# Kernel optimization log

Hardware: AMD Instinct MI355X
Metric: run time of the kernel (lower is better)

Reference implementation:

```python
import jax, jax.numpy as jnp
import numpy as np

N = 100000   # nodes
E = 1600000  # edges (avg degree 16)
D = 64       # out_channels (in_channels == out_channels, so no zero-padding step)
L = 2        # GatedGraphConv num_layers


def setup_inputs() -> dict:
    key = jax.random.key(0)
    ks = jax.random.split(key, 11)
    w = lambda k, shape: jax.random.normal(k, shape, jnp.float32) * 0.05
    return {
        "x": jax.random.normal(ks[0], (N, D), jnp.float32),
        "edge_index": jax.random.randint(ks[1], (2, E), 0, N, dtype=jnp.int64),
        "conv_w": w(ks[2], (L, D, D)),        # GatedGraphConv per-layer message weight
        "gru_w_ih": w(ks[3], (3 * D, D)),     # GRUCell input->hidden (r|z|n)
        "gru_w_hh": w(ks[4], (3 * D, D)),     # GRUCell hidden->hidden (r|z|n)
        "gru_b_ih": w(ks[5], (3 * D,)),
        "gru_b_hh": w(ks[6], (3 * D,)),
        "lin_w": w(ks[7], (D, D)),            # nn.Linear(out, out)
        "lin_b": w(ks[8], (D,)),
        "attn_w": w(ks[9], (1, D)),           # nn.Linear(out, 1)
        "attn_b": w(ks[10], (1,)),
    }


def reference(x, edge_index, conv_w, gru_w_ih, gru_w_hh, gru_b_ih, gru_b_hh,
              lin_w, lin_b, attn_w, attn_b):
    src, dst = edge_index[0], edge_index[1]
    h = x  # in_channels == out_channels -> no padding
    for i in range(L):
        m = h @ conv_w[i]  # [N, D] transformed messages
        # gather at source nodes, scatter-add into target nodes
        agg = jax.ops.segment_sum(m[src], dst, num_segments=N)  # [N, D]
        # GRUCell(agg, h)
        gi = agg @ gru_w_ih.T + gru_b_ih  # [N, 3D]
        gh = h @ gru_w_hh.T + gru_b_hh    # [N, 3D]
        i_r, i_z, i_n = jnp.split(gi, 3, axis=1)
        h_r, h_z, h_n = jnp.split(gh, 3, axis=1)
        r = jax.nn.sigmoid(i_r + h_r)
        z = jax.nn.sigmoid(i_z + h_z)
        n = jnp.tanh(i_n + r * h_n)
        h = (1.0 - z) * n + z * h
    y = jax.nn.relu(h) @ lin_w.T + lin_b                 # [N, D]
    attn = jax.nn.softmax(y @ attn_w.T + attn_b, axis=0) # [N, 1], softmax over nodes
    return (attn * y).sum(axis=0, keepdims=True)          # [1, D]
```

## Files before the change

kernel.cpp:

```cpp
#include <hip/hip_runtime.h>


typedef __attribute__((ext_vector_type(8))) short s8v;
typedef __attribute__((ext_vector_type(4))) float f32x4;

#define CSR_CAP 12288
#define HSTR 136
#define LSTR 72

__device__ __forceinline__ unsigned short f32_bf16_rn(float x) {
  unsigned u = __float_as_uint(x);
  u += 0x7FFF + ((u >> 16) & 1);
  return (unsigned short)(u >> 16);
}

__device__ __forceinline__ int wave_incl_scan(int v, int lane) {
#pragma unroll
  for (int d = 1; d < 64; d <<= 1) {
    int u = __shfl_up(v, d);
    if (lane >= d) v += u;
  }
  return v;
}

__device__ __forceinline__ int detect_is64(const int* ei, int E) {
  int nz = 0;
  int lim = (E < 512) ? E : 512;
  for (int i = threadIdx.x; i < lim; i += blockDim.x)
    nz |= (ei[2 * i + 1] != 0);
  return __syncthreads_or(nz) ? 0 : 1;
}

__device__ __forceinline__ void load_edge(const int* ei, int E, int is64,
                                          int e, int& s, int& d) {
  if (is64) { s = ei[2 * e]; d = ei[2 * (E + e)]; }
  else      { s = ei[e];     d = ei[E + e]; }
}

__global__ __launch_bounds__(256) void count_kernel(
    const int* __restrict__ ei, int E,
    int* __restrict__ G, int P, int perBlk, int NB) {
  __shared__ int hist[512];
  int tid = threadIdx.x, b = blockIdx.x;
  for (int i = tid; i < 512; i += 256) hist[i] = 0;
  int is64 = detect_is64(ei, E);
  __syncthreads();
  int e0 = b * perBlk, e1 = min(e0 + perBlk, E);
  for (int e = e0 + tid; e < e1; e += 256) {
    int s, d; load_edge(ei, E, is64, e, s, d);
    atomicAdd(&hist[d >> 8], 1);
  }
  __syncthreads();
  for (int i = tid; i < P; i += 256) G[i * NB + b] = hist[i];
}

__global__ __launch_bounds__(256) void scan2a(int* __restrict__ G,
                                              int* __restrict__ total, int NB) {
  __shared__ int wsum[4];
  int p = blockIdx.x, tid = threadIdx.x, lane = tid & 63, wv = tid >> 6;
  int v = G[p * NB + tid];
  int incl = wave_incl_scan(v, lane);
  if (lane == 63) wsum[wv] = incl;
  __syncthreads();
  if (tid == 0) {
    int a = wsum[0], b2 = wsum[1], c = wsum[2], d = wsum[3];
    total[p] = a + b2 + c + d;
    wsum[0] = 0; wsum[1] = a; wsum[2] = a + b2; wsum[3] = a + b2 + c;
  }
  __syncthreads();
  G[p * NB + tid] = incl - v + wsum[wv];
}

__global__ void scan2b(const int* __restrict__ total, int* __restrict__ partStart,
                       int P) {
  int lane = threadIdx.x;
  int running = 0;
  for (int base = 0; base < P; base += 64) {
    int idx = base + lane;
    int v = (idx < P) ? total[idx] : 0;
    int incl = wave_incl_scan(v, lane);
    int tot = __shfl(incl, 63);
    if (idx < P) partStart[idx] = running + incl - v;
    running += tot;
  }
  if (lane == 0) partStart[P] = running;
}

__global__ __launch_bounds__(256) void scatter_kernel(
    const int* __restrict__ ei, int E,
    const int* __restrict__ G, const int* __restrict__ partStart,
    int* __restrict__ bucket, int P, int perBlk, int NB) {
  __shared__ int cur[512];
  int tid = threadIdx.x, b = blockIdx.x;
  int is64 = detect_is64(ei, E);
  for (int i = tid; i < P; i += 256) cur[i] = partStart[i] + G[i * NB + b];
  __syncthreads();
  int e0 = b * perBlk, e1 = min(e0 + perBlk, E);
  for (int e = e0 + tid; e < e1; e += 256) {
    int s, d; load_edge(ei, E, is64, e, s, d);
    int pos = atomicAdd(&cur[d >> 8], 1);
    bucket[pos] = ((d & 255) << 17) | s;
  }
}

__global__ __launch_bounds__(256) void buildcsr_kernel(
    const int* __restrict__ partStart, const int* __restrict__ bucket,
    int* __restrict__ row_ptr, int* __restrict__ col, int N) {
  __shared__ int stage[CSR_CAP];
  __shared__ int hist[256];
  __shared__ int cur[256];
  __shared__ int wsum[4];
  int p = blockIdx.x, tid = threadIdx.x;
  int beg = partStart[p], end = partStart[p + 1];
  int cnt = end - beg;
  int base = p << 8;
  hist[tid] = 0;
  __syncthreads();
  bool staged = (cnt <= CSR_CAP);
  if (staged) {
    for (int i = tid; i < cnt; i += 256) {
      int v = bucket[beg + i];
      stage[i] = v;
      atomicAdd(&hist[(v >> 17) & 255], 1);
    }
  } else {
    for (int i = tid; i < cnt; i += 256)
      atomicAdd(&hist[(bucket[beg + i] >> 17) & 255], 1);
  }
  __syncthreads();
  int lane = tid & 63, wv = tid >> 6;
  int v = hist[tid];
  int incl = wave_incl_scan(v, lane);
  if (lane == 63) wsum[wv] = incl;
  __syncthreads();
  if (tid == 0) {
    int s0 = wsum[0], s1 = wsum[1], s2 = wsum[2];
    wsum[0] = 0; wsum[1] = s0; wsum[2] = s0 + s1; wsum[3] = s0 + s1 + s2;
  }
  __syncthreads();
  int excl = incl - v + wsum[wv];
  cur[tid] = beg + excl;
  if (base + tid < N) {
    if (tid == 0) row_ptr[base] = beg;
    row_ptr[base + tid + 1] = beg + excl + v;
  }
  __syncthreads();
  if (staged) {
    for (int i = tid; i < cnt; i += 256) {
      int v2 = stage[i];
      int pos = atomicAdd(&cur[(v2 >> 17) & 255], 1);
      col[pos] = v2 & 0x1FFFF;
    }
  } else {
    for (int i = tid; i < cnt; i += 256) {
      int v2 = bucket[beg + i];
      int pos = atomicAdd(&cur[(v2 >> 17) & 255], 1);
      col[pos] = v2 & 0x1FFFF;
    }
  }
}

__global__ void wprep_kernel(const float* __restrict__ conv_w,
                             const float* __restrict__ w_ih,
                             const float* __restrict__ whh,
                             const float* __restrict__ lin_w,
                             unsigned short* __restrict__ Bt,
                             unsigned short* __restrict__ Lt) {
  int idx = blockIdx.x * blockDim.x + threadIdx.x;
  if (idx < 65536) {
    int l = idx >> 15;
    int rr = idx & 32767;
    int c = rr >> 7, p = rr & 127;
    int g = c >> 6, ch = c & 63;
    float val = 0.f;
    if (p < 64) {
      int j = (g == 0) ? ch : (g == 1) ? 64 + ch : (g == 2) ? 128 + ch : -1;
      if (j >= 0) {
        const float* C = conv_w + l * 4096 + p * 64;
        const float* W = w_ih + j * 64;
#pragma unroll 8
        for (int k = 0; k < 64; k++) val += C[k] * W[k];
      }
    } else {
      int q = p - 64;
      if (g == 0)      val = whh[ch * 64 + q];
      else if (g == 1) val = whh[(64 + ch) * 64 + q];
      else if (g == 3) val = whh[(128 + ch) * 64 + q];
    }
    unsigned short hi = f32_bf16_rn(val);
    float fh = __uint_as_float((unsigned)hi << 16);
    unsigned short lo = f32_bf16_rn(val - fh);
    size_t base = (size_t)l * 65536;
    Bt[base + (size_t)c * 128 + p] = hi;
    Bt[base + 32768 + (size_t)c * 128 + p] = lo;
  } else if (idx < 65536 + 4096) {
    int i2 = idx - 65536;
    float val = lin_w[i2];
    unsigned short hi = f32_bf16_rn(val);
    float fh = __uint_as_float((unsigned)hi << 16);
    unsigned short lo = f32_bf16_rn(val - fh);
    Lt[i2] = hi;
    Lt[4096 + i2] = lo;
  }
}

__global__ __launch_bounds__(256) void cvt16_kernel(
    const float* __restrict__ in, unsigned short* __restrict__ out, int n8) {
  int idx = blockIdx.x * blockDim.x + threadIdx.x;
  if (idx >= n8) return;
  const float4* p = (const float4*)(in + (size_t)idx * 8);
  float4 v0 = p[0], v1 = p[1];
  uint4 o;
  o.x = (unsigned)f32_bf16_rn(v0.x) | ((unsigned)f32_bf16_rn(v0.y) << 16);
  o.y = (unsigned)f32_bf16_rn(v0.z) | ((unsigned)f32_bf16_rn(v0.w) << 16);
  o.z = (unsigned)f32_bf16_rn(v1.x) | ((unsigned)f32_bf16_rn(v1.y) << 16);
  o.w = (unsigned)f32_bf16_rn(v1.z) | ((unsigned)f32_bf16_rn(v1.w) << 16);
  *(uint4*)(out + (size_t)idx * 8) = o;
}

__device__ __forceinline__ void acc_u4(const uint4& r, float* a) {
  a[0] += __uint_as_float(r.x << 16);
  a[1] += __uint_as_float(r.x & 0xFFFF0000u);
  a[2] += __uint_as_float(r.y << 16);
  a[3] += __uint_as_float(r.y & 0xFFFF0000u);
  a[4] += __uint_as_float(r.z << 16);
  a[5] += __uint_as_float(r.z & 0xFFFF0000u);
  a[6] += __uint_as_float(r.w << 16);
  a[7] += __uint_as_float(r.w & 0xFFFF0000u);
}

__global__ __launch_bounds__(256, 2) void gemm_gru_kernel(
    const unsigned short* __restrict__ src16, const int* __restrict__ row_ptr,
    const int* __restrict__ col, const float* __restrict__ hin,
    float* __restrict__ hout, unsigned short* __restrict__ hb16,
    const unsigned short* __restrict__ bt,
    const float* __restrict__ b_ih, const float* __restrict__ b_hh,
    int N, int ntiles, int wb16) {
  __shared__ short Ahi[64 * HSTR];
  __shared__ short Alo[64 * LSTR];
  const int tid = threadIdx.x;
  const int lane = tid & 63, w = tid >> 6;
  const int l15 = lane & 15, ko = (lane >> 4) * 8;

  s8v Bh[4][4], Bl[4][4];
  {
    const int colc = 16 * w + l15;
#pragma unroll
    for (int c = 0; c < 4; c++)
#pragma unroll
      for (int kk = 0; kk < 4; kk++) {
        size_t o = (size_t)(64 * c + colc) * 128 + kk * 32 + ko;
        Bh[c][kk] = *(const s8v*)(bt + o);
        Bl[c][kk] = *(const s8v*)(bt + 32768 + o);
      }
  }
  const int ch = 16 * w + l15;
  const float br = b_ih[ch] + b_hh[ch];
  const float bz = b_ih[64 + ch] + b_hh[64 + ch];
  const float bin_ = b_ih[128 + ch];
  const float bhn = b_hh[128 + ch];
  const int q4 = (lane >> 4) * 4;
  const int g = tid >> 2, qc = tid & 3;

  for (int tile = blockIdx.x; tile < ntiles; tile += gridDim.x) {
    const int nb = tile * 64;
    const int node = nb + g;
    {
      float a[16];
#pragma unroll
      for (int i = 0; i < 16; i++) a[i] = 0.f;
      if (node < N) {
        int beg = row_ptr[node], end = row_ptr[node + 1];
        int e = beg;
        for (; e + 2 <= end; e += 2) {
          const unsigned short* b0 = src16 + (size_t)col[e] * 64 + qc * 16;
          const unsigned short* b1 = src16 + (size_t)col[e + 1] * 64 + qc * 16;
          uint4 r0 = *(const uint4*)b0;
          uint4 r1 = *(const uint4*)(b0 + 8);
          uint4 r2 = *(const uint4*)b1;
          uint4 r3 = *(const uint4*)(b1 + 8);
          acc_u4(r0, a); acc_u4(r1, a + 8);
          acc_u4(r2, a); acc_u4(r3, a + 8);
        }
        if (e < end) {
          const unsigned short* b0 = src16 + (size_t)col[e] * 64 + qc * 16;
          uint4 r0 = *(const uint4*)b0;
          uint4 r1 = *(const uint4*)(b0 + 8);
          acc_u4(r0, a); acc_u4(r1, a + 8);
        }
      }
      s8v sv0, sv1;
#pragma unroll
      for (int i = 0; i < 8; i++) {
        sv0[i] = (short)f32_bf16_rn(a[i]);
        sv1[i] = (short)f32_bf16_rn(a[8 + i]);
      }
      short* sh = &Ahi[g * HSTR + qc * 16];
      *(s8v*)sh = sv0;
      *(s8v*)(sh + 8) = sv1;
    }
    {
      f32x4 v[4];
      if (node < N) {
#pragma unroll
        for (int i = 0; i < 4; i++)
          v[i] = *(const f32x4*)(hin + (size_t)node * 64 + qc * 16 + 4 * i);
      } else {
#pragma unroll
        for (int i = 0; i < 4; i++) v[i] = (f32x4)(0.f);
      }
      s8v hv0, hv1, lv0, lv1;
#pragma unroll
      for (int i = 0; i < 8; i++) {
        float x0 = v[i >> 2][i & 3];
        float x1 = v[2 + (i >> 2)][i & 3];
        unsigned short hb0 = f32_bf16_rn(x0);
        unsigned short hb1 = f32_bf16_rn(x1);
        hv0[i] = (short)hb0;
        hv1[i] = (short)hb1;
        lv0[i] = (short)f32_bf16_rn(x0 - __uint_as_float((unsigned)hb0 << 16));
        lv1[i] = (short)f32_bf16_rn(x1 - __uint_as_float((unsigned)hb1 << 16));
      }
      short* hh = &Ahi[g * HSTR + 64 + qc * 16];
      *(s8v*)hh = hv0;
      *(s8v*)(hh + 8) = hv1;
      short* hl = &Alo[g * LSTR + qc * 16];
      *(s8v*)hl = lv0;
      *(s8v*)(hl + 8) = lv1;
    }
    __syncthreads();

    f32x4 acc[4][4];
#pragma unroll
    for (int m = 0; m < 4; m++)
#pragma unroll
      for (int c = 0; c < 4; c++) acc[m][c] = (f32x4)(0.f);

#pragma unroll
    for (int m = 0; m < 4; m++) {
      const short* arh = &Ahi[(16 * m + l15) * HSTR + ko];
      const short* arl = &Alo[(16 * m + l15) * LSTR + ko];
#pragma unroll
      for (int kk = 0; kk < 4; kk++) {
        s8v a_h = *(const s8v*)(arh + kk * 32);
#pragma unroll
        for (int c = 0; c < 4; c++) {
          acc[m][c] = __builtin_amdgcn_mfma_f32_16x16x32_bf16(a_h, Bh[c][kk], acc[m][c], 0, 0, 0);
          acc[m][c] = __builtin_amdgcn_mfma_f32_16x16x32_bf16(a_h, Bl[c][kk], acc[m][c], 0, 0, 0);
        }
        if (kk >= 2) {
          s8v a_l = *(const s8v*)(arl + (kk - 2) * 32);
#pragma unroll
          for (int c = 0; c < 4; c++)
            acc[m][c] = __builtin_amdgcn_mfma_f32_16x16x32_bf16(a_l, Bh[c][kk], acc[m][c], 0, 0, 0);
        }
      }
    }

#pragma unroll
    for (int m = 0; m < 4; m++) {
#pragma unroll
      for (int gg = 0; gg < 4; gg++) {
        int loc = 16 * m + q4 + gg;
        int nd = nb + loc;
        if (nd < N) {
          unsigned hi = (unsigned short)Ahi[loc * HSTR + 64 + ch];
          unsigned lo = (unsigned short)Alo[loc * LSTR + ch];
          float hold = __uint_as_float(hi << 16) + __uint_as_float(lo << 16);
          float rr = 1.f / (1.f + __expf(-(acc[m][0][gg] + br)));
          float zz = 1.f / (1.f + __expf(-(acc[m][1][gg] + bz)));
          float narg = acc[m][2][gg] + bin_ + rr * (acc[m][3][gg] + bhn);
          narg = fminf(fmaxf(narg, -15.f), 15.f);
          float t = __expf(2.f * narg);
          float nn = (t - 1.f) / (t + 1.f);
          float hv = (1.f - zz) * nn + zz * hold;
          hout[(size_t)nd * 64 + ch] = hv;
          if (wb16) hb16[(size_t)nd * 64 + ch] = f32_bf16_rn(hv);
        }
      }
    }
    __syncthreads();
  }
}

__global__ __launch_bounds__(256, 2) void final_mfma(
    const float* __restrict__ h, const unsigned short* __restrict__ Lt,
    const float* __restrict__ lin_b, const float* __restrict__ attn_w,
    const float* __restrict__ attn_b, float* __restrict__ partials,
    int N, int ntiles) {
  __shared__ short Alds[2 * 64 * 72];
  __shared__ float red[4][64];
  __shared__ float pl[64];
  const int tid = threadIdx.x;
  const int lane = tid & 63, w = tid >> 6;
  const int l15 = lane & 15, ko = (lane >> 4) * 8;
  const int q = lane >> 4;

  s8v Lh[2], Ll[2];
  const int col = 16 * w + l15;
#pragma unroll
  for (int kk = 0; kk < 2; kk++) {
    Lh[kk] = *(const s8v*)(Lt + (size_t)col * 64 + kk * 32 + ko);
    Ll[kk] = *(const s8v*)(Lt + 4096 + (size_t)col * 64 + kk * 32 + ko);
  }
  const float lb = lin_b[col];
  const float aw = attn_w[col];
  const float ab = attn_b[0];
  const int sr = tid >> 2, part = tid & 3;

  float accS = 0.f;
  float accY = 0.f;

  for (int tile = blockIdx.x; tile < ntiles; tile += gridDim.x) {
    const int nb = tile * 64;
    {
      int node = nb + sr;
      f32x4 v[4];
      if (node < N) {
#pragma unroll
        for (int i = 0; i < 4; i++)
          v[i] = *(const f32x4*)(h + (size_t)node * 64 + part * 16 + 4 * i);
      } else {
#pragma unroll
        for (int i = 0; i < 4; i++) v[i] = (f32x4)(0.f);
      }
      short* ah = &Alds[sr * 72 + part * 16];
#pragma unroll
      for (int i2 = 0; i2 < 2; i2++) {
        s8v hv, lv;
#pragma unroll
        for (int e = 0; e < 8; e++) {
          float x = fmaxf(v[i2 * 2 + (e >> 2)][e & 3], 0.f);
          unsigned short hb = f32_bf16_rn(x);
          float fh = __uint_as_float((unsigned)hb << 16);
          unsigned short lo2 = f32_bf16_rn(x - fh);
          hv[e] = (short)hb;
          lv[e] = (short)lo2;
        }
        *(s8v*)(ah + i2 * 8) = hv;
        *(s8v*)(ah + 64 * 72 + i2 * 8) = lv;
      }
    }
    __syncthreads();

    f32x4 acc[4];
#pragma unroll
    for (int m = 0; m < 4; m++) acc[m] = (f32x4)(0.f);
#pragma unroll
    for (int m = 0; m < 4; m++) {
      const short* arow = &Alds[(16 * m + l15) * 72 + ko];
#pragma unroll
      for (int kk = 0; kk < 2; kk++) {
        s8v a_h = *(const s8v*)(arow + kk * 32);
        s8v a_l = *(const s8v*)(arow + 64 * 72 + kk * 32);
        acc[m] = __builtin_amdgcn_mfma_f32_16x16x32_bf16(a_h, Lh[kk], acc[m], 0, 0, 0);
        acc[m] = __builtin_amdgcn_mfma_f32_16x16x32_bf16(a_h, Ll[kk], acc[m], 0, 0, 0);
        acc[m] = __builtin_amdgcn_mfma_f32_16x16x32_bf16(a_l, Lh[kk], acc[m], 0, 0, 0);
      }
    }
    __syncthreads();

    float cc[4][4];
#pragma unroll
    for (int m = 0; m < 4; m++)
#pragma unroll
      for (int g = 0; g < 4; g++) cc[m][g] = (acc[m][g] + lb) * aw;
#pragma unroll
    for (int off = 1; off <= 8; off <<= 1)
#pragma unroll
      for (int m = 0; m < 4; m++)
#pragma unroll
        for (int g = 0; g < 4; g++) cc[m][g] += __shfl_xor(cc[m][g], off);
    if (l15 == 0) {
#pragma unroll
      for (int m = 0; m < 4; m++)
#pragma unroll
        for (int g = 0; g < 4; g++) red[w][16 * m + 4 * q + g] = cc[m][g];
    }
    __syncthreads();
    if (tid < 64) {
      float t = red[0][tid] + red[1][tid] + red[2][tid] + red[3][tid] + ab;
      float p = (nb + tid < N) ? __expf(t) : 0.f;
      pl[tid] = p;
      accS += p;
    }
    __syncthreads();
#pragma unroll
    for (int m = 0; m < 4; m++)
#pragma unroll
      for (int g = 0; g < 4; g++)
        accY += pl[16 * m + 4 * q + g] * (acc[m][g] + lb);
  }

  accY += __shfl_xor(accY, 16);
  accY += __shfl_xor(accY, 32);
  if (lane < 16) partials[(size_t)blockIdx.x * 66 + 16 * w + lane] = accY;
  if (w == 0) {
    float s = accS;
#pragma unroll
    for (int off = 1; off < 64; off <<= 1) s += __shfl_xor(s, off);
    if (lane == 0) partials[(size_t)blockIdx.x * 66 + 64] = s;
  }
}

__global__ void final_p2(const float* __restrict__ partials,
                         float* __restrict__ out, int nb) {
  __shared__ float red[16][65];
  int tid = threadIdx.x;
  int j = tid & 63, grp = tid >> 6;
  float sy = 0.f, ss = 0.f;
  for (int b = grp; b < nb; b += 16) {
    sy += partials[b * 66 + j];
    if (j == 0) ss += partials[b * 66 + 64];
  }
  red[grp][j] = sy;
  if (j == 0) red[grp][64] = ss;
  __syncthreads();
  if (tid < 64) {
    float Y = 0.f, S = 0.f;
#pragma unroll
    for (int i = 0; i < 16; i++) { Y += red[i][tid]; S += red[i][64]; }
    out[tid] = Y / S;
  }
}

extern "C" void kernel_launch(void* const* d_in, const int* in_sizes, int n_in,
                              void* d_out, int out_size, void* d_ws, size_t ws_size,
                              hipStream_t stream) {
  const float* x       = (const float*)d_in[0];
  const int*   ei      = (const int*)d_in[1];
  const float* conv_w  = (const float*)d_in[2];
  const float* gw_ih   = (const float*)d_in[3];
  const float* gw_hh   = (const float*)d_in[4];
  const float* gb_ih   = (const float*)d_in[5];
  const float* gb_hh   = (const float*)d_in[6];
  const float* lin_w   = (const float*)d_in[7];
  const float* lin_b   = (const float*)d_in[8];
  const float* attn_w  = (const float*)d_in[9];
  const float* attn_b  = (const float*)d_in[10];
  float* out = (float*)d_out;

  const int N = in_sizes[0] / 64;
  const int E = in_sizes[1] / 2;
  const int P  = (N + 255) >> 8;
  const int NB = 256;
  const int perBlk = (E + NB - 1) / NB;

  char* ws = (char*)d_ws;
  size_t off = 0;
  auto alloc = [&](size_t bytes) {
    void* p = ws + off;
    off = (off + bytes + 255) & ~(size_t)255;
    return p;
  };
  int*   G         = (int*)alloc((size_t)P * NB * 4);
  int*   total     = (int*)alloc((size_t)P * 4);
  int*   partStart = (int*)alloc((size_t)(P + 1) * 4);
  int*   bucket    = (int*)alloc((size_t)E * 4);
  int*   row_ptr   = (int*)alloc((size_t)(N + 1) * 4);
  int*   colb      = (int*)alloc((size_t)E * 4);
  unsigned short* Bt  = (unsigned short*)alloc(2 * 2 * 256 * 128 * 2);
  unsigned short* Lt  = (unsigned short*)alloc(2 * 4096 * 2);
  unsigned short* b16x = (unsigned short*)alloc((size_t)N * 64 * 2);
  unsigned short* b16h = (unsigned short*)alloc((size_t)N * 64 * 2);
  float* hbuf      = (float*)alloc((size_t)N * 64 * 4);
  float* partials  = (float*)alloc(1024 * 66 * 4);
  if (off > ws_size) return;

  count_kernel<<<NB, 256, 0, stream>>>(ei, E, G, P, perBlk, NB);
  scan2a<<<P, 256, 0, stream>>>(G, total, NB);
  scan2b<<<1, 64, 0, stream>>>(total, partStart, P);
  scatter_kernel<<<NB, 256, 0, stream>>>(ei, E, G, partStart, bucket, P, perBlk, NB);
  buildcsr_kernel<<<P, 256, 0, stream>>>(partStart, bucket, row_ptr, colb, N);
  wprep_kernel<<<(65536 + 4096 + 255) / 256, 256, 0, stream>>>(conv_w, gw_ih, gw_hh,
                                                               lin_w, Bt, Lt);
  int n8 = (N * 64) / 8;
  cvt16_kernel<<<(n8 + 255) / 256, 256, 0, stream>>>(x, b16x, n8);

  int ntiles = (N + 63) / 64;
  gemm_gru_kernel<<<512, 256, 0, stream>>>(b16x, row_ptr, colb, x, hbuf, b16h,
                                           Bt, gb_ih, gb_hh, N, ntiles, 1);
  gemm_gru_kernel<<<512, 256, 0, stream>>>(b16h, row_ptr, colb, hbuf, hbuf, b16h,
                                           Bt + 65536, gb_ih, gb_hh, N, ntiles, 0);
  final_mfma<<<512, 256, 0, stream>>>(hbuf, Lt, lin_b, attn_w, attn_b, partials, N, ntiles);
  final_p2<<<1, 1024, 0, stream>>>(partials, out, 512);
}
```

Baseline: 235.0 us.

## Drop bf16 lo-part of weights, interleave gate columns, widen GRU blocks to 512 threads

The fused gather+GEMM+GRU kernel now uses a single bf16 copy of the combined weights instead of a hi/lo split, which halves the MFMA count and the B-fragment registers. Weight columns are interleaved per channel (r,z,n_i,n_h) so each wave owns 32 columns, and the gate values are gathered to one lane via shuffles for the GRU epilogue. Blocks grow to 512 threads with 8 threads per node in the gather, unrolled by 4 edges, to raise occupancy and memory-level parallelism. Weight precision drops (bf16 only), and in the epilogue only a quarter of lanes do the work, with scattered scalar stores.

```diff
diff --git a/kernel.cpp b/kernel.cpp
--- a/kernel.cpp
+++ b/kernel.cpp
@@ -170,8 +170,8 @@
   if (idx < 65536) {
     int l = idx >> 15;
     int rr = idx & 32767;
-    int c = rr >> 7, p = rr & 127;
-    int g = c >> 6, ch = c & 63;
+    int cp = rr >> 7, p = rr & 127;
+    int ch = cp >> 2, g = cp & 3;
     float val = 0.f;
     if (p < 64) {
       int j = (g == 0) ? ch : (g == 1) ? 64 + ch : (g == 2) ? 128 + ch : -1;
@@ -187,12 +187,7 @@
       else if (g == 1) val = whh[(64 + ch) * 64 + q];
       else if (g == 3) val = whh[(128 + ch) * 64 + q];
     }
-    unsigned short hi = f32_bf16_rn(val);
-    float fh = __uint_as_float((unsigned)hi << 16);
-    unsigned short lo = f32_bf16_rn(val - fh);
-    size_t base = (size_t)l * 65536;
-    Bt[base + (size_t)c * 128 + p] = hi;
-    Bt[base + 32768 + (size_t)c * 128 + p] = lo;
+    Bt[(size_t)l * 32768 + (size_t)cp * 128 + p] = f32_bf16_rn(val);
   } else if (idx < 65536 + 4096) {
     int i2 = idx - 65536;
     float val = lin_w[i2];
@@ -229,7 +224,7 @@
   a[7] += __uint_as_float(r.w & 0xFFFF0000u);
 }
 
-__global__ __launch_bounds__(256, 2) void gemm_gru_kernel(
+__global__ __launch_bounds__(512, 4) void gemm_gru_kernel(
     const unsigned short* __restrict__ src16, const int* __restrict__ row_ptr,
     const int* __restrict__ col, const float* __restrict__ hin,
     float* __restrict__ hout, unsigned short* __restrict__ hb16,
@@ -242,99 +237,74 @@
   const int lane = tid & 63, w = tid >> 6;
   const int l15 = lane & 15, ko = (lane >> 4) * 8;
 
-  s8v Bh[4][4], Bl[4][4];
-  {
-    const int colc = 16 * w + l15;
-#pragma unroll
-    for (int c = 0; c < 4; c++)
-#pragma unroll
-      for (int kk = 0; kk < 4; kk++) {
-        size_t o = (size_t)(64 * c + colc) * 128 + kk * 32 + ko;
-        Bh[c][kk] = *(const s8v*)(bt + o);
-        Bl[c][kk] = *(const s8v*)(bt + 32768 + o);
-      }
-  }
-  const int ch = 16 * w + l15;
-  const float br = b_ih[ch] + b_hh[ch];
-  const float bz = b_ih[64 + ch] + b_hh[64 + ch];
-  const float bin_ = b_ih[128 + ch];
-  const float bhn = b_hh[128 + ch];
-  const int q4 = (lane >> 4) * 4;
-  const int g = tid >> 2, qc = tid & 3;
+  s8v Bf[2][4];
+#pragma unroll
+  for (int ct = 0; ct < 2; ct++)
+#pragma unroll
+    for (int kk = 0; kk < 4; kk++)
+      Bf[ct][kk] = *(const s8v*)(bt + (size_t)(32 * w + 16 * ct + l15) * 128 +
+                                 kk * 32 + ko);
+
+  const int ch0 = 8 * w + (l15 >> 2);
+  const int ch1 = ch0 + 4;
+  const float br0 = b_ih[ch0] + b_hh[ch0], br1 = b_ih[ch1] + b_hh[ch1];
+  const float bz0 = b_ih[64 + ch0] + b_hh[64 + ch0], bz1 = b_ih[64 + ch1] + b_hh[64 + ch1];
+  const float bi0 = b_ih[128 + ch0], bi1 = b_ih[128 + ch1];
+  const float bn0 = b_hh[128 + ch0], bn1 = b_hh[128 + ch1];
+
+  const int g = tid >> 3, qc = tid & 7;
 
   for (int tile = blockIdx.x; tile < ntiles; tile += gridDim.x) {
     const int nb = tile * 64;
     const int node = nb + g;
     {
-      float a[16];
-#pragma unroll
-      for (int i = 0; i < 16; i++) a[i] = 0.f;
+      float a[8];
+#pragma unroll
+      for (int i = 0; i < 8; i++) a[i] = 0.f;
       if (node < N) {
         int beg = row_ptr[node], end = row_ptr[node + 1];
         int e = beg;
-        for (; e + 2 <= end; e += 2) {
-          const unsigned short* b0 = src16 + (size_t)col[e] * 64 + qc * 16;
-          const unsigned short* b1 = src16 + (size_t)col[e + 1] * 64 + qc * 16;
-          uint4 r0 = *(const uint4*)b0;
-          uint4 r1 = *(const uint4*)(b0 + 8);
-          uint4 r2 = *(const uint4*)b1;
-          uint4 r3 = *(const uint4*)(b1 + 8);
-          acc_u4(r0, a); acc_u4(r1, a + 8);
-          acc_u4(r2, a); acc_u4(r3, a + 8);
+        for (; e + 4 <= end; e += 4) {
+          uint4 r0 = *(const uint4*)(src16 + (size_t)col[e] * 64 + qc * 8);
+          uint4 r1 = *(const uint4*)(src16 + (size_t)col[e + 1] * 64 + qc * 8);
+          uint4 r2 = *(const uint4*)(src16 + (size_t)col[e + 2] * 64 + qc * 8);
+          uint4 r3 = *(const uint4*)(src16 + (size_t)col[e + 3] * 64 + qc * 8);
+          acc_u4(r0, a); acc_u4(r1, a); acc_u4(r2, a); acc_u4(r3, a);
         }
-        if (e < end) {
-          const unsigned short* b0 = src16 + (size_t)col[e] * 64 + qc * 16;
-          uint4 r0 = *(const uint4*)b0;
-          uint4 r1 = *(const uint4*)(b0 + 8);
-          acc_u4(r0, a); acc_u4(r1, a + 8);
+        for (; e < end; e++) {
+          uint4 r0 = *(const uint4*)(src16 + (size_t)col[e] * 64 + qc * 8);
+          acc_u4(r0, a);
         }
       }
-      s8v sv0, sv1;
+      s8v sv;
+#pragma unroll
+      for (int i = 0; i < 8; i++) sv[i] = (short)f32_bf16_rn(a[i]);
+      *(s8v*)&Ahi[g * HSTR + qc * 8] = sv;
+    }
+    {
+      f32x4 v0 = (f32x4)(0.f), v1 = (f32x4)(0.f);
+      if (node < N) {
+        v0 = *(const f32x4*)(hin + (size_t)node * 64 + qc * 8);
+        v1 = *(const f32x4*)(hin + (size_t)node * 64 + qc * 8 + 4);
+      }
+      s8v hv, lv;
 #pragma unroll
       for (int i = 0; i < 8; i++) {
-        sv0[i] = (short)f32_bf16_rn(a[i]);
-        sv1[i] = (short)f32_bf16_rn(a[8 + i]);
-      }
-      short* sh = &Ahi[g * HSTR + qc * 16];
-      *(s8v*)sh = sv0;
-      *(s8v*)(sh + 8) = sv1;
-    }
-    {
-      f32x4 v[4];
-      if (node < N) {
-#pragma unroll
-        for (int i = 0; i < 4; i++)
-          v[i] = *(const f32x4*)(hin + (size_t)node * 64 + qc * 16 + 4 * i);
-      } else {
-#pragma unroll
-        for (int i = 0; i < 4; i++) v[i] = (f32x4)(0.f);
-      }
-      s8v hv0, hv1, lv0, lv1;
-#pragma unroll
-      for (int i = 0; i < 8; i++) {
-        float x0 = v[i >> 2][i & 3];
-        float x1 = v[2 + (i >> 2)][i & 3];
-        unsigned short hb0 = f32_bf16_rn(x0);
-        unsigned short hb1 = f32_bf16_rn(x1);
-        hv0[i] = (short)hb0;
-        hv1[i] = (short)hb1;
-        lv0[i] = (short)f32_bf16_rn(x0 - __uint_as_float((unsigned)hb0 << 16));
-        lv1[i] = (short)f32_bf16_rn(x1 - __uint_as_float((unsigned)hb1 << 16));
-      }
-      short* hh = &Ahi[g * HSTR + 64 + qc * 16];
-      *(s8v*)hh = hv0;
-      *(s8v*)(hh + 8) = hv1;
-      short* hl = &Alo[g * LSTR + qc * 16];
-      *(s8v*)hl = lv0;
-      *(s8v*)(hl + 8) = lv1;
+        float x = (i < 4) ? v0[i] : v1[i - 4];
+        unsigned short hb = f32_bf16_rn(x);
+        hv[i] = (short)hb;
+        lv[i] = (short)f32_bf16_rn(x - __uint_as_float((unsigned)hb << 16));
+      }
+      *(s8v*)&Ahi[g * HSTR + 64 + qc * 8] = hv;
+      *(s8v*)&Alo[g * LSTR + qc * 8] = lv;
     }
     __syncthreads();
 
-    f32x4 acc[4][4];
+    f32x4 acc[4][2];
 #pragma unroll
     for (int m = 0; m < 4; m++)
 #pragma unroll
-      for (int c = 0; c < 4; c++) acc[m][c] = (f32x4)(0.f);
+      for (int ct = 0; ct < 2; ct++) acc[m][ct] = (f32x4)(0.f);
 
 #pragma unroll
     for (int m = 0; m < 4; m++) {
@@ -344,38 +314,48 @@
       for (int kk = 0; kk < 4; kk++) {
         s8v a_h = *(const s8v*)(arh + kk * 32);
 #pragma unroll
-        for (int c = 0; c < 4; c++) {
-          acc[m][c] = __builtin_amdgcn_mfma_f32_16x16x32_bf16(a_h, Bh[c][kk], acc[m][c], 0, 0, 0);
-          acc[m][c] = __builtin_amdgcn_mfma_f32_16x16x32_bf16(a_h, Bl[c][kk], acc[m][c], 0, 0, 0);
-        }
+        for (int ct = 0; ct < 2; ct++)
+          acc[m][ct] = __builtin_amdgcn_mfma_f32_16x16x32_bf16(a_h, Bf[ct][kk], acc[m][ct], 0, 0, 0);
         if (kk >= 2) {
           s8v a_l = *(const s8v*)(arl + (kk - 2) * 32);
 #pragma unroll
-          for (int c = 0; c < 4; c++)
-            acc[m][c] = __builtin_amdgcn_mfma_f32_16x16x32_bf16(a_l, Bh[c][kk], acc[m][c], 0, 0, 0);
+          for (int ct = 0; ct < 2; ct++)
+            acc[m][ct] = __builtin_amdgcn_mfma_f32_16x16x32_bf16(a_l, Bf[ct][kk], acc[m][ct], 0, 0, 0);
         }
       }
     }
 
+    const int srcb = lane & ~3;
 #pragma unroll
     for (int m = 0; m < 4; m++) {
 #pragma unroll
-      for (int gg = 0; gg < 4; gg++) {
-        int loc = 16 * m + q4 + gg;
-        int nd = nb + loc;
-        if (nd < N) {
-          unsigned hi = (unsigned short)Ahi[loc * HSTR + 64 + ch];
-          unsigned lo = (unsigned short)Alo[loc * LSTR + ch];
-          float hold = __uint_as_float(hi << 16) + __uint_as_float(lo << 16);
-          float rr = 1.f / (1.f + __expf(-(acc[m][0][gg] + br)));
-          float zz = 1.f / (1.f + __expf(-(acc[m][1][gg] + bz)));
-          float narg = acc[m][2][gg] + bin_ + rr * (acc[m][3][gg] + bhn);
-          narg = fminf(fmaxf(narg, -15.f), 15.f);
-          float t = __expf(2.f * narg);
-          float nn = (t - 1.f) / (t + 1.f);
-          float hv = (1.f - zz) * nn + zz * hold;
-          hout[(size_t)nd * 64 + ch] = hv;
-          if (wb16) hb16[(size_t)nd * 64 + ch] = f32_bf16_rn(hv);
+      for (int ct = 0; ct < 2; ct++) {
+#pragma unroll
+        for (int gg = 0; gg < 4; gg++) {
+          float a = acc[m][ct][gg];
+          float r_ = __shfl(a, srcb);
+          float z_ = __shfl(a, srcb | 1);
+          float i_ = __shfl(a, srcb | 2);
+          float hn_ = __shfl(a, srcb | 3);
+          if ((lane & 3) == 0) {
+            int loc = 16 * m + (lane >> 4) * 4 + gg;
+            int nd = nb + loc;
+            if (nd < N) {
+              int ch = ct ? ch1 : ch0;
+              unsigned hi = (unsigned short)Ahi[loc * HSTR + 64 + ch];
+              unsigned lo = (unsigned short)Alo[loc * LSTR + ch];
+              float hold = __uint_as_float(hi << 16) + __uint_as_float(lo << 16);
+              float rr = 1.f / (1.f + __expf(-(r_ + (ct ? br1 : br0))));
+              float zz = 1.f / (1.f + __expf(-(z_ + (ct ? bz1 : bz0))));
+              float narg = i_ + (ct ? bi1 : bi0) + rr * (hn_ + (ct ? bn1 : bn0));
+              narg = fminf(fmaxf(narg, -15.f), 15.f);
+              float t = __expf(2.f * narg);
+              float nn = (t - 1.f) / (t + 1.f);
+              float hv = (1.f - zz) * nn + zz * hold;
+              hout[(size_t)nd * 64 + ch] = hv;
+              if (wb16) hb16[(size_t)nd * 64 + ch] = f32_bf16_rn(hv);
+            }
+          }
         }
       }
     }
@@ -559,7 +539,7 @@
   int*   bucket    = (int*)alloc((size_t)E * 4);
   int*   row_ptr   = (int*)alloc((size_t)(N + 1) * 4);
   int*   colb      = (int*)alloc((size_t)E * 4);
-  unsigned short* Bt  = (unsigned short*)alloc(2 * 2 * 256 * 128 * 2);
+  unsigned short* Bt  = (unsigned short*)alloc(2 * 256 * 128 * 2);
   unsigned short* Lt  = (unsigned short*)alloc(2 * 4096 * 2);
   unsigned short* b16x = (unsigned short*)alloc((size_t)N * 64 * 2);
   unsigned short* b16h = (unsigned short*)alloc((size_t)N * 64 * 2);
@@ -578,10 +558,10 @@
   cvt16_kernel<<<(n8 + 255) / 256, 256, 0, stream>>>(x, b16x, n8);
 
   int ntiles = (N + 63) / 64;
-  gemm_gru_kernel<<<512, 256, 0, stream>>>(b16x, row_ptr, colb, x, hbuf, b16h,
+  gemm_gru_kernel<<<512, 512, 0, stream>>>(b16x, row_ptr, colb, x, hbuf, b16h,
                                            Bt, gb_ih, gb_hh, N, ntiles, 1);
-  gemm_gru_kernel<<<512, 256, 0, stream>>>(b16h, row_ptr, colb, hbuf, hbuf, b16h,
-                                           Bt + 65536, gb_ih, gb_hh, N, ntiles, 0);
+  gemm_gru_kernel<<<512, 512, 0, stream>>>(b16h, row_ptr, colb, hbuf, hbuf, b16h,
+                                           Bt + 32768, gb_ih, gb_hh, N, ntiles, 0);
   final_mfma<<<512, 256, 0, stream>>>(hbuf, Lt, lin_b, attn_w, attn_b, partials, N, ntiles);
   final_p2<<<1, 1024, 0, stream>>>(partials, out, 512);
 }
```

Result: slower. 261.3 us (+11.2%).
